# Optimization experiments

Measured on AMD Instinct MI355X. Metric: run time of the kernel, lower is better.

Reference implementation:

```python
import jax, jax.numpy as jnp
import numpy as np

B, T, D = 32, 8192, 256
CTX = 128

def setup_inputs() -> dict:
    key = jax.random.key(0)
    kx, kw, ku = jax.random.split(key, 3)
    X = jax.random.normal(kx, (B, T, D), dtype=jnp.float32)
    # keras 'uniform' initializer: U(-0.05, 0.05)
    W = jax.random.uniform(kw, (D, CTX), dtype=jnp.float32, minval=-0.05, maxval=0.05)
    u = jax.random.uniform(ku, (CTX, 1), dtype=jnp.float32, minval=-0.05, maxval=0.05)
    return {"X": X, "W": W, "u": u}

def reference(X, W, u):
    # additive attention over time axis
    u_tw = jnp.tanh(jnp.einsum('btd,dc->btc', X, W))        # (B,T,CTX)
    scores = jnp.einsum('btc,co->bt', u_tw, u)              # (B,T)
    att = jax.nn.softmax(scores, axis=1)                    # (B,T)
    # weighted sum over time, no repeated-elements materialization
    return jnp.einsum('bt,btd->bd', att, X)                 # (B,D)
```

## Files before the change

### kernel.cpp

```cpp
#include <hip/hip_runtime.h>
#include <stdint.h>

#define B_N   32
#define T_N   8192
#define D_N   256
#define CTX_N 128
#define TB    32
#define CPB   8
#define ROWS_PB (TB*CPB)
#define BLK_PER_B (T_N/ROWS_PB)
#define NBLOCKS (B_N*BLK_PER_B)
#define XP    264
#define SPW   12

typedef unsigned short u16;
typedef unsigned int   u32;
typedef __attribute__((ext_vector_type(8))) short bf16x8;
typedef __attribute__((ext_vector_type(8))) unsigned short u16x8;
typedef __attribute__((ext_vector_type(4))) float f32x4;

__device__ __forceinline__ u16 f2bf(float f) {
  u32 u = __float_as_uint(f);
  return (u16)((u + 0x7FFFu + ((u >> 16) & 1u)) >> 16);
}
__device__ __forceinline__ float bf2f(u16 h) {
  return __uint_as_float(((u32)h) << 16);
}
__device__ __forceinline__ float fast_tanh(float x) {
  float e = __expf(2.0f * x);
  return (e - 1.0f) * __builtin_amdgcn_rcpf(e + 1.0f);
}
__device__ __forceinline__ float rr16_add(float v) {
  int x;
  x = __builtin_amdgcn_update_dpp(0, __float_as_int(v), 0x128, 0xF, 0xF, true); v += __int_as_float(x);
  x = __builtin_amdgcn_update_dpp(0, __float_as_int(v), 0x124, 0xF, 0xF, true); v += __int_as_float(x);
  x = __builtin_amdgcn_update_dpp(0, __float_as_int(v), 0x122, 0xF, 0xF, true); v += __int_as_float(x);
  x = __builtin_amdgcn_update_dpp(0, __float_as_int(v), 0x121, 0xF, 0xF, true); v += __int_as_float(x);
  return v;
}

__global__ void prep_w(const float* __restrict__ W, u16* __restrict__ Wt) {
  int c = blockIdx.x;
  int d = threadIdx.x;
  Wt[c * D_N + d] = f2bf(W[d * CTX_N + c]);
}

__global__ __launch_bounds__(512, 4)
void attn_main(const float* __restrict__ X, const u16* __restrict__ Wt,
               const float* __restrict__ u,
               float* __restrict__ blk_o, float* __restrict__ blk_l) {
  __shared__ u16   Xl[2][TB][XP];
  __shared__ __align__(16) float s_part[TB][SPW];
  __shared__ float l_part[16];

  const int tid = threadIdx.x;
  const int w   = tid >> 6;
  const int l   = tid & 63;
  const int l15 = l & 15;
  const int lg  = l >> 4;

  const int blk  = blockIdx.x;
  const int b    = blk >> 5;
  const int rowB = (blk & (BLK_PER_B - 1)) * ROWS_PB;
  const float* Xbase = X + ((size_t)b * T_N + rowB) * D_N;

  bf16x8 bw[8];
  {
    const u16* wp = Wt + (w * 16 + l15) * D_N + lg * 8;
    #pragma unroll
    for (int kk = 0; kk < 8; ++kk) bw[kk] = *(const bf16x8*)(wp + kk * 32);
  }
  const float uc = u[w * 16 + l15];

  const int srow = tid >> 4;
  const int scol = (tid & 15) << 4;

  float4 pf0, pf1, pf2, pf3;
  {
    const float* sp = Xbase + (size_t)srow * D_N + scol;
    pf0 = ((const float4*)sp)[0]; pf1 = ((const float4*)sp)[1];
    pf2 = ((const float4*)sp)[2]; pf3 = ((const float4*)sp)[3];
  }

  const int g     = tid >> 5;
  const int slice = tid & 31;
  float o8[8] = {0,0,0,0,0,0,0,0};
  float l_run = 0.f;

  for (int c = 0; c < CPB; ++c) {
    const int cur = c & 1;

    u16x8 s0, s1;
    s0[0]=f2bf(pf0.x); s0[1]=f2bf(pf0.y); s0[2]=f2bf(pf0.z); s0[3]=f2bf(pf0.w);
    s0[4]=f2bf(pf1.x); s0[5]=f2bf(pf1.y); s0[6]=f2bf(pf1.z); s0[7]=f2bf(pf1.w);
    s1[0]=f2bf(pf2.x); s1[1]=f2bf(pf2.y); s1[2]=f2bf(pf2.z); s1[3]=f2bf(pf2.w);
    s1[4]=f2bf(pf3.x); s1[5]=f2bf(pf3.y); s1[6]=f2bf(pf3.z); s1[7]=f2bf(pf3.w);
    *(u16x8*)&Xl[cur][srow][scol]     = s0;
    *(u16x8*)&Xl[cur][srow][scol + 8] = s1;

    if (c + 1 < CPB) {
      const float* sp = Xbase + ((size_t)(c + 1) * TB + srow) * D_N + scol;
      pf0 = ((const float4*)sp)[0]; pf1 = ((const float4*)sp)[1];
      pf2 = ((const float4*)sp)[2]; pf3 = ((const float4*)sp)[3];
    }

    asm volatile("s_waitcnt lgkmcnt(0)" ::: "memory");
    __builtin_amdgcn_s_barrier();
    asm volatile("" ::: "memory");

    const u16* Xc = &Xl[cur][0][0];
    f32x4 acc0 = {0,0,0,0}, acc1 = {0,0,0,0};
    #pragma unroll
    for (int kk = 0; kk < 8; ++kk) {
      bf16x8 a0 = *(const bf16x8*)(Xc + l15 * XP + kk * 32 + lg * 8);
      bf16x8 a1 = *(const bf16x8*)(Xc + (16 + l15) * XP + kk * 32 + lg * 8);
      acc0 = __builtin_amdgcn_mfma_f32_16x16x32_bf16(a0, bw[kk], acc0, 0, 0, 0);
      acc1 = __builtin_amdgcn_mfma_f32_16x16x32_bf16(a1, bw[kk], acc1, 0, 0, 0);
    }
    #pragma unroll
    for (int r = 0; r < 4; ++r) {
      float v0 = rr16_add(uc * fast_tanh(acc0[r]));
      float v1 = rr16_add(uc * fast_tanh(acc1[r]));
      if (l15 == 0) {
        s_part[lg * 4 + r][w]      = v0;
        s_part[16 + lg * 4 + r][w] = v1;
      }
    }
    asm volatile("s_waitcnt lgkmcnt(0)" ::: "memory");
    __builtin_amdgcn_s_barrier();
    asm volatile("" ::: "memory");

    float4 sa0 = *(const float4*)&s_part[2 * g][0];
    float4 sa1 = *(const float4*)&s_part[2 * g][4];
    float4 sb0 = *(const float4*)&s_part[2 * g + 1][0];
    float4 sb1 = *(const float4*)&s_part[2 * g + 1][4];
    float st0 = sa0.x; st0 += sa0.y; st0 += sa0.z; st0 += sa0.w;
    st0 += sa1.x; st0 += sa1.y; st0 += sa1.z; st0 += sa1.w;
    float st1 = sb0.x; st1 += sb0.y; st1 += sb0.z; st1 += sb0.w;
    st1 += sb1.x; st1 += sb1.y; st1 += sb1.z; st1 += sb1.w;
    float p0 = __expf(st0), p1 = __expf(st1);
    if (slice == 0) l_run += p0 + p1;
    u16x8 x0 = *(const u16x8*)&Xl[cur][2 * g][slice * 8];
    u16x8 x1 = *(const u16x8*)&Xl[cur][2 * g + 1][slice * 8];
    #pragma unroll
    for (int j = 0; j < 8; ++j) o8[j] += p0 * bf2f(x0[j]) + p1 * bf2f(x1[j]);
  }

  asm volatile("s_waitcnt lgkmcnt(0)" ::: "memory");
  __builtin_amdgcn_s_barrier();
  asm volatile("" ::: "memory");
  float* comb = (float*)&Xl[0][0][0];
  #pragma unroll
  for (int j = 0; j < 8; ++j) comb[g * 256 + slice * 8 + j] = o8[j];
  if (slice == 0) l_part[g] = l_run;
  asm volatile("s_waitcnt lgkmcnt(0)" ::: "memory");
  __builtin_amdgcn_s_barrier();
  asm volatile("" ::: "memory");
  if (tid < 256) {
    float o = 0.f;
    #pragma unroll
    for (int g2 = 0; g2 < 16; ++g2) o += comb[g2 * 256 + tid];
    blk_o[(size_t)blk * D_N + tid] = o;
  }
  if (tid == 0) {
    float L = 0.f;
    #pragma unroll
    for (int g2 = 0; g2 < 16; ++g2) L += l_part[g2];
    blk_l[blk] = L;
  }
}

__global__ __launch_bounds__(256)
void finalize(const float* __restrict__ blk_o, const float* __restrict__ blk_l,
              float* __restrict__ out) {
  const int b = blockIdx.x, d = threadIdx.x;
  float o = 0.f, L = 0.f;
  for (int i = 0; i < BLK_PER_B; ++i) {
    o += blk_o[(size_t)(b * BLK_PER_B + i) * D_N + d];
    L += blk_l[b * BLK_PER_B + i];
  }
  out[b * D_N + d] = o / L;
}

extern "C" void kernel_launch(void* const* d_in, const int* in_sizes, int n_in,
                              void* d_out, int out_size, void* d_ws, size_t ws_size,
                              hipStream_t stream) {
  const float* X = (const float*)d_in[0];
  const float* W = (const float*)d_in[1];
  const float* u = (const float*)d_in[2];
  float* out = (float*)d_out;

  u16*   Wt    = (u16*)d_ws;
  float* blk_o = (float*)((char*)d_ws + 65536);
  float* blk_l = (float*)((char*)d_ws + 65536 + (size_t)NBLOCKS * D_N * 4);

  prep_w<<<CTX_N, D_N, 0, stream>>>(W, Wt);
  attn_main<<<NBLOCKS, 512, 0, stream>>>(X, Wt, u, blk_o, blk_l);
  finalize<<<B_N, 256, 0, stream>>>(blk_o, blk_l, out);
}
```

Before: 59.61 us.

## Software-pipeline weighted-sum one chunk behind scores to drop a barrier

Defers the softmax-weighted accumulation for chunk c-1 into iteration c, right after the single per-iteration barrier. This removes the second barrier per chunk. To keep data valid, the X tile buffer goes from double to triple buffering and the score partials are double-buffered. LDS use rises (three 32x264 bf16 tiles), which could lower occupancy at 4 blocks per CU.

Measured after the change: 58.76 us. No clear change (-1.4%).

```diff
diff --git a/kernel.cpp b/kernel.cpp
--- a/kernel.cpp
+++ b/kernel.cpp
@@ -49,8 +49,8 @@
 void attn_main(const float* __restrict__ X, const u16* __restrict__ Wt,
                const float* __restrict__ u,
                float* __restrict__ blk_o, float* __restrict__ blk_l) {
-  __shared__ u16   Xl[2][TB][XP];
-  __shared__ __align__(16) float s_part[TB][SPW];
+  __shared__ u16   Xl[3][TB][XP];
+  __shared__ __align__(16) float s_part[2][TB][SPW];
   __shared__ float l_part[16];
 
   const int tid = threadIdx.x;
@@ -87,16 +87,34 @@
   float o8[8] = {0,0,0,0,0,0,0,0};
   float l_run = 0.f;
 
+  auto wsum = [&](int m) {
+    const int pb = m % 3, sp = m & 1;
+    float4 sa0 = *(const float4*)&s_part[sp][2 * g][0];
+    float4 sa1 = *(const float4*)&s_part[sp][2 * g][4];
+    float4 sb0 = *(const float4*)&s_part[sp][2 * g + 1][0];
+    float4 sb1 = *(const float4*)&s_part[sp][2 * g + 1][4];
+    float st0 = sa0.x; st0 += sa0.y; st0 += sa0.z; st0 += sa0.w;
+    st0 += sa1.x; st0 += sa1.y; st0 += sa1.z; st0 += sa1.w;
+    float st1 = sb0.x; st1 += sb0.y; st1 += sb0.z; st1 += sb0.w;
+    st1 += sb1.x; st1 += sb1.y; st1 += sb1.z; st1 += sb1.w;
+    float p0 = __expf(st0), p1 = __expf(st1);
+    if (slice == 0) l_run += p0 + p1;
+    u16x8 x0 = *(const u16x8*)&Xl[pb][2 * g][slice * 8];
+    u16x8 x1 = *(const u16x8*)&Xl[pb][2 * g + 1][slice * 8];
+    #pragma unroll
+    for (int j = 0; j < 8; ++j) o8[j] += p0 * bf2f(x0[j]) + p1 * bf2f(x1[j]);
+  };
+
   for (int c = 0; c < CPB; ++c) {
-    const int cur = c & 1;
+    const int cb = c % 3;
 
     u16x8 s0, s1;
     s0[0]=f2bf(pf0.x); s0[1]=f2bf(pf0.y); s0[2]=f2bf(pf0.z); s0[3]=f2bf(pf0.w);
     s0[4]=f2bf(pf1.x); s0[5]=f2bf(pf1.y); s0[6]=f2bf(pf1.z); s0[7]=f2bf(pf1.w);
     s1[0]=f2bf(pf2.x); s1[1]=f2bf(pf2.y); s1[2]=f2bf(pf2.z); s1[3]=f2bf(pf2.w);
     s1[4]=f2bf(pf3.x); s1[5]=f2bf(pf3.y); s1[6]=f2bf(pf3.z); s1[7]=f2bf(pf3.w);
-    *(u16x8*)&Xl[cur][srow][scol]     = s0;
-    *(u16x8*)&Xl[cur][srow][scol + 8] = s1;
+    *(u16x8*)&Xl[cb][srow][scol]     = s0;
+    *(u16x8*)&Xl[cb][srow][scol + 8] = s1;
 
     if (c + 1 < CPB) {
       const float* sp = Xbase + ((size_t)(c + 1) * TB + srow) * D_N + scol;
@@ -108,7 +126,9 @@
     __builtin_amdgcn_s_barrier();
     asm volatile("" ::: "memory");
 
-    const u16* Xc = &Xl[cur][0][0];
+    if (c >= 1) wsum(c - 1);
+
+    const u16* Xc = &Xl[cb][0][0];
     f32x4 acc0 = {0,0,0,0}, acc1 = {0,0,0,0};
     #pragma unroll
     for (int kk = 0; kk < 8; ++kk) {
@@ -122,29 +142,16 @@
       float v0 = rr16_add(uc * fast_tanh(acc0[r]));
       float v1 = rr16_add(uc * fast_tanh(acc1[r]));
       if (l15 == 0) {
-        s_part[lg * 4 + r][w]      = v0;
-        s_part[16 + lg * 4 + r][w] = v1;
+        s_part[c & 1][lg * 4 + r][w]      = v0;
+        s_part[c & 1][16 + lg * 4 + r][w] = v1;
       }
     }
-    asm volatile("s_waitcnt lgkmcnt(0)" ::: "memory");
-    __builtin_amdgcn_s_barrier();
-    asm volatile("" ::: "memory");
-
-    float4 sa0 = *(const float4*)&s_part[2 * g][0];
-    float4 sa1 = *(const float4*)&s_part[2 * g][4];
-    float4 sb0 = *(const float4*)&s_part[2 * g + 1][0];
-    float4 sb1 = *(const float4*)&s_part[2 * g + 1][4];
-    float st0 = sa0.x; st0 += sa0.y; st0 += sa0.z; st0 += sa0.w;
-    st0 += sa1.x; st0 += sa1.y; st0 += sa1.z; st0 += sa1.w;
-    float st1 = sb0.x; st1 += sb0.y; st1 += sb0.z; st1 += sb0.w;
-    st1 += sb1.x; st1 += sb1.y; st1 += sb1.z; st1 += sb1.w;
-    float p0 = __expf(st0), p1 = __expf(st1);
-    if (slice == 0) l_run += p0 + p1;
-    u16x8 x0 = *(const u16x8*)&Xl[cur][2 * g][slice * 8];
-    u16x8 x1 = *(const u16x8*)&Xl[cur][2 * g + 1][slice * 8];
-    #pragma unroll
-    for (int j = 0; j < 8; ++j) o8[j] += p0 * bf2f(x0[j]) + p1 * bf2f(x1[j]);
-  }
+  }
+
+  asm volatile("s_waitcnt lgkmcnt(0)" ::: "memory");
+  __builtin_amdgcn_s_barrier();
+  asm volatile("" ::: "memory");
+  wsum(CPB - 1);
 
   asm volatile("s_waitcnt lgkmcnt(0)" ::: "memory");
   __builtin_amdgcn_s_barrier();
```
